# Kernel tuning notes

Hardware: AMD Instinct MI355X
Metric: run time of the kernel (lower is better)

The kernel has to match this reference:

```python
import jax, jax.numpy as jnp
import numpy as np

N = 16384   # nodes (atoms)
E = 262144  # edges (avg degree 16)
C = 64      # hidden channels per degree
H = 8       # attention heads
L = 4       # layers
R = 32      # radial MLP hidden
AED = 32    # atom embedding dim
TED = 32    # timestep embedding dim
NT = 1000   # num diffusion timesteps
NA = 16     # num atom types
DIN = AED + TED


def _sinusoidal(seq_len, dim):
    pos = np.arange(seq_len, dtype=np.float32)[:, None]
    dims = np.arange(dim, dtype=np.float32)[None, :]
    ang = pos / 10000.0 ** (2.0 * np.floor(dims / 2.0) / dim)
    emb = np.zeros((seq_len, dim), dtype=np.float32)
    emb[:, 0::2] = np.sin(ang[:, 0::2])
    emb[:, 1::2] = np.cos(ang[:, 1::2])
    return jnp.asarray(emb)


def setup_inputs() -> dict:
    key = jax.random.key(0)
    ks = jax.random.split(key, 20)
    def w(k, shape, fan_in):
        return jax.random.normal(k, shape, jnp.float32) / np.float32(np.sqrt(fan_in))
    return {
        'coordinates': jax.random.normal(ks[0], (N, 3), jnp.float32),
        'embed_table': w(ks[1], (NA, AED), 1.0),
        't_emb': _sinusoidal(NT, TED),
        'Win_s': w(ks[2], (DIN, C), DIN),
        'Win_v': w(ks[3], (1, C), 1.0),
        'Wq_s': w(ks[4], (L, C, C), C),
        'Wq_v': w(ks[5], (L, C, C), C),
        'Wk_s': w(ks[6], (L, C, C), C),
        'Wk_v': w(ks[7], (L, C, C), C),
        'R_W1': w(ks[8], (L, 1, R), 1.0),
        'R_b1': jnp.zeros((L, R), jnp.float32),
        'R_W2': w(ks[9], (L, R, H * 8), R),
        'R_b2': jnp.zeros((L, H * 8), jnp.float32),
        'Wo_s': w(ks[10], (L, C, C), C),
        'Wo_v': w(ks[11], (L, C, C), C),
        'Wout_v': w(ks[12], (C, 1), C),
        'atoms': jax.random.randint(ks[13], (N,), 0, NA),
        'src': jax.random.randint(ks[14], (E,), 0, N),
        'dst': jax.random.randint(ks[15], (E,), 0, N),
        't': 500,
    }


def _forward(coordinates, embed_table, t_emb, Win_s, Win_v, Wq_s, Wq_v, Wk_s, Wk_v,
             R_W1, R_b1, R_W2, R_b2, Wo_s, Wo_v, Wout_v, atoms, src, dst, t):
    n = coordinates.shape[0]
    Ch = C // H
    # center coordinates (as in wrapper)
    x = coordinates - coordinates.mean(axis=0, keepdims=True)
    # degree-0 input: atom embedding ++ timestep embedding
    s = jnp.concatenate([embed_table[atoms], jnp.broadcast_to(t_emb[t], (n, TED))], axis=-1)
    s = s @ Win_s                                        # [N, C] scalars
    # degree-1 input: coordinates (1 channel), lifted to C channels
    v = jnp.einsum('nkd,kc->ncd', x[:, None, :], Win_v)  # [N, C, 3] vectors
    # edge geometry (spherical-harmonic basis up to l=1: Y0=const, Y1 ~ rhat)
    rel = x[dst] - x[src]
    d = jnp.sqrt(jnp.sum(rel * rel, axis=-1) + 1e-12)    # [E]
    rhat = rel / d[:, None]                              # [E, 3]
    rh = rhat[:, None, None, :]                          # [E,1,1,3]
    for l in range(L):
        # radial network -> per-head CG-path weights (key/value x {0->0,1->0,1->1,0->1})
        rad = (jax.nn.relu(d[:, None] @ R_W1[l] + R_b1[l]) @ R_W2[l] + R_b2[l]).reshape(-1, H, 8)
        k_s = (s @ Wk_s[l])[src].reshape(-1, H, Ch)                          # [E,H,Ch]
        k_v = jnp.einsum('ecd,cf->efd', v[src], Wk_v[l]).reshape(-1, H, Ch, 3)
        vdotr = jnp.einsum('ehcd,ed->ehc', k_v, rhat)                        # 1x1 -> 0 path
        key_s = rad[..., 0:1] * k_s + rad[..., 1:2] * vdotr
        key_v = rad[..., 2:3, None] * k_v + rad[..., 3:4, None] * k_s[..., None] * rh
        val_s = rad[..., 4:5] * k_s + rad[..., 5:6] * vdotr
        val_v = rad[..., 6:7, None] * k_v + rad[..., 7:8, None] * k_s[..., None] * rh
        q_s = (s @ Wq_s[l]).reshape(n, H, Ch)[dst]
        q_v = jnp.einsum('ncd,cf->nfd', v, Wq_v[l]).reshape(n, H, Ch, 3)[dst]
        # invariant attention logits over incoming edges
        logit = ((q_s * key_s).sum(-1) + (q_v * key_v).sum((-1, -2))) / np.float32(np.sqrt(Ch))
        m = jax.lax.stop_gradient(jax.ops.segment_max(logit, dst, num_segments=n))
        a = jnp.exp(logit - m[dst])
        denom = jax.ops.segment_sum(a, dst, num_segments=n)
        alpha = a / (denom[dst] + 1e-9)                                      # [E,H]
        agg_s = jax.ops.segment_sum(alpha[..., None] * val_s, dst, num_segments=n).reshape(n, C)
        agg_v = jax.ops.segment_sum(alpha[..., None, None] * val_v, dst, num_segments=n).reshape(n, C, 3)
        # self-interaction + residual + equivariant nonlinearity
        s = jax.nn.silu(s + agg_s @ Wo_s[l])
        vr = v + jnp.einsum('ncd,cf->nfd', agg_v, Wo_v[l])
        v = vr * jax.nn.sigmoid(jnp.sum(vr * vr, axis=-1, keepdims=True))    # norm gate
    # fiber_out degree-1 with 1 channel -> updated coordinates
    return jnp.einsum('ncd,ck->nkd', v, Wout_v)[:, 0, :]                     # [N, 3]


def reference(coordinates, embed_table, t_emb, Win_s, Win_v, Wq_s, Wq_v, Wk_s, Wk_v,
              R_W1, R_b1, R_W2, R_b2, Wo_s, Wo_v, Wout_v, atoms, src, dst, t):
    return _forward(coordinates, embed_table, t_emb, Win_s, Win_v, Wq_s, Wq_v, Wk_s, Wk_v,
                    R_W1, R_b1, R_W2, R_b2, Wo_s, Wo_v, Wout_v, atoms, src, dst, t)
```

## Files before the change

kernel.cpp:

```cpp
#include <hip/hip_runtime.h>
#include <math.h>

#define NN 16384
#define NE 262144

constexpr size_t OFF_PART  = 0;
constexpr size_t OFF_MEAN  = 256;
constexpr size_t OFF_T     = 512;
constexpr size_t OFF_BIAS  = 1536;
constexpr size_t OFF_S     = 2048;
constexpr size_t OFF_V     = OFF_S     + (size_t)NN * 64;
constexpr size_t OFF_GEOM  = OFF_V     + (size_t)NN * 192;
constexpr size_t OFF_GEOMC = OFF_GEOM  + (size_t)NE * 4;
constexpr size_t OFF_QS    = OFF_GEOMC + (size_t)NE * 4;
constexpr size_t OFF_KS    = OFF_QS    + (size_t)NN * 64;
constexpr size_t OFF_QV    = OFF_KS    + (size_t)NN * 64;
constexpr size_t OFF_KV    = OFF_QV    + (size_t)NN * 192;
constexpr size_t OFF_RAD   = OFF_KV    + (size_t)NN * 192;
constexpr size_t OFF_INT   = OFF_RAD   + (size_t)NE * 64;
constexpr size_t I_ROWPTR  = OFF_INT;
constexpr size_t I_CURSOR  = OFF_INT + 16640;
constexpr size_t I_SRCC    = I_CURSOR + (size_t)NN;

static __device__ __forceinline__ double sigmoidd_(double x) {
  return 1.0 / (1.0 + exp(-x));
}

static __device__ __forceinline__ double fast_exp(double x) {
  x = fmax(x, -708.0);
  double y = x * 1.4426950408889634074;
  double k = rint(y);
  double r = fma(k, -6.93147180369123816490e-01, x);
  r = fma(k, -1.90821492927058770002e-10, r);
  double p = 2.755731922398589e-7;
  p = fma(p, r, 2.7557319223985893e-6);
  p = fma(p, r, 2.48015873015873016e-5);
  p = fma(p, r, 1.98412698412698413e-4);
  p = fma(p, r, 1.38888888888888889e-3);
  p = fma(p, r, 8.33333333333333333e-3);
  p = fma(p, r, 4.16666666666666667e-2);
  p = fma(p, r, 1.66666666666666667e-1);
  p = fma(p, r, 0.5);
  p = fma(p, r, 1.0);
  p = fma(p, r, 1.0);
  long long ki = (long long)k;
  double sc = __longlong_as_double((unsigned long long)(1023LL + ki) << 52);
  return p * sc;
}

__global__ void k_mean_partial(const float* __restrict__ coords, float* __restrict__ partials) {
  __shared__ double sm[3][256];
  int tid = threadIdx.x;
  int n = blockIdx.x * 256 + tid;
  sm[0][tid] = (double)coords[n * 3 + 0];
  sm[1][tid] = (double)coords[n * 3 + 1];
  sm[2][tid] = (double)coords[n * 3 + 2];
  __syncthreads();
  for (int off = 128; off > 0; off >>= 1) {
    if (tid < off) {
      sm[0][tid] += sm[0][tid + off];
      sm[1][tid] += sm[1][tid + off];
      sm[2][tid] += sm[2][tid + off];
    }
    __syncthreads();
  }
  if (tid == 0) {
    partials[blockIdx.x * 3 + 0] = (float)sm[0][0];
    partials[blockIdx.x * 3 + 1] = (float)sm[1][0];
    partials[blockIdx.x * 3 + 2] = (float)sm[2][0];
  }
}

__global__ void k_mean_final(const float* __restrict__ partials, float* __restrict__ mean) {
  int lane = threadIdx.x;
  double s0 = (double)partials[lane * 3 + 0];
  double s1 = (double)partials[lane * 3 + 1];
  double s2 = (double)partials[lane * 3 + 2];
  for (int off = 32; off > 0; off >>= 1) {
    s0 += __shfl_xor(s0, off);
    s1 += __shfl_xor(s1, off);
    s2 += __shfl_xor(s2, off);
  }
  if (lane == 0) {
    mean[0] = (float)(s0 * (1.0 / (double)NN));
    mean[1] = (float)(s1 * (1.0 / (double)NN));
    mean[2] = (float)(s2 * (1.0 / (double)NN));
  }
}

__global__ void k_prep_T(const float* __restrict__ embed, const float* __restrict__ t_emb,
                         const float* __restrict__ Win_s, const int* __restrict__ tptr,
                         float* __restrict__ T, float* __restrict__ bias) {
  int f = threadIdx.x;
  int tv = tptr[0];
  double b = 0.0;
  for (int k = 0; k < 32; ++k)
    b = fma((double)t_emb[tv * 32 + k], (double)Win_s[(32 + k) * 64 + f], b);
  bias[f] = (float)b;
  for (int a = 0; a < 16; ++a) {
    double acc = 0.0;
    for (int k = 0; k < 32; ++k)
      acc = fma((double)embed[a * 32 + k], (double)Win_s[k * 64 + f], acc);
    T[a * 64 + f] = (float)acc;
  }
}

__global__ void k_init_nodes(const float* __restrict__ coords, const float* __restrict__ mean,
                             const int* __restrict__ atoms, const float* __restrict__ T,
                             const float* __restrict__ bias, const float* __restrict__ Win_v,
                             float* __restrict__ S, float* __restrict__ V) {
  int id = blockIdx.x * 256 + threadIdx.x;
  int n = id >> 6, c = id & 63;
  double x0 = (double)coords[n * 3 + 0] - (double)mean[0];
  double x1 = (double)coords[n * 3 + 1] - (double)mean[1];
  double x2 = (double)coords[n * 3 + 2] - (double)mean[2];
  int a = atoms[n];
  S[n * 64 + c] = T[a * 64 + c] + bias[c];
  double w = (double)Win_v[c];
  V[(n * 64 + c) * 3 + 0] = (float)(x0 * w);
  V[(n * 64 + c) * 3 + 1] = (float)(x1 * w);
  V[(n * 64 + c) * 3 + 2] = (float)(x2 * w);
}

__global__ void k_edge_geom(const float* __restrict__ coords, const int* __restrict__ src,
                            const int* __restrict__ dst, float4* __restrict__ geom,
                            int* __restrict__ count) {
  int e = blockIdx.x * 256 + threadIdx.x;
  int se = src[e], de = dst[e];
  double rx = (double)coords[de * 3 + 0] - (double)coords[se * 3 + 0];
  double ry = (double)coords[de * 3 + 1] - (double)coords[se * 3 + 1];
  double rz = (double)coords[de * 3 + 2] - (double)coords[se * 3 + 2];
  double d2 = rx * rx + ry * ry + rz * rz + 1e-12;
  double dd = sqrt(d2);
  double inv = 1.0 / dd;
  geom[e] = make_float4((float)dd, (float)(rx * inv), (float)(ry * inv), (float)(rz * inv));
  atomicAdd(&count[de], 1);
}

__global__ void k_scan(int* count_cursor, int* rowptr) {
  __shared__ int buf[256];
  __shared__ int carry_s;
  int tid = threadIdx.x;
  if (tid == 0) carry_s = 0;
  __syncthreads();
  for (int base = 0; base < NN; base += 256) {
    int idx = base + tid;
    int val = count_cursor[idx];
    buf[tid] = val;
    __syncthreads();
    int incl = val;
    for (int off = 1; off < 256; off <<= 1) {
      int t = (tid >= off) ? buf[tid - off] : 0;
      __syncthreads();
      incl += t;
      buf[tid] = incl;
      __syncthreads();
    }
    int excl = carry_s + incl - val;
    rowptr[idx] = excl;
    count_cursor[idx] = excl;
    __syncthreads();
    if (tid == 255) carry_s += incl;
    __syncthreads();
  }
  if (tid == 0) rowptr[NN] = carry_s;
}

__global__ void k_scatter(const int* __restrict__ dst, const int* __restrict__ src,
                          const float4* __restrict__ geom, int* __restrict__ cursor,
                          int* __restrict__ srcc, float4* __restrict__ geomc) {
  int e = blockIdx.x * 256 + threadIdx.x;
  int de = dst[e];
  int pos = atomicAdd(&cursor[de], 1);
  srcc[pos] = src[e];
  geomc[pos] = geom[e];
}

__global__ void k_rad(const float4* __restrict__ geomc,
                      const float* __restrict__ R_W1, const float* __restrict__ R_b1,
                      const float* __restrict__ R_W2, const float* __restrict__ R_b2,
                      float* __restrict__ radc, int l) {
  __shared__ float2 w1b1[32];
  __shared__ float b2s[64];
  __shared__ float w2s[2048];
  for (int i = threadIdx.x; i < 2048; i += 256) w2s[i] = R_W2[l * 2048 + i];
  if (threadIdx.x < 64) b2s[threadIdx.x] = R_b2[l * 64 + threadIdx.x];
  if (threadIdx.x < 32)
    w1b1[threadIdx.x] = make_float2(R_W1[l * 32 + threadIdx.x], R_b1[l * 32 + threadIdx.x]);
  __syncthreads();
  int lane = threadIdx.x & 63;
  float w2col[32];
#pragma unroll
  for (int r = 0; r < 32; ++r) w2col[r] = w2s[r * 64 + lane];
  double b2v = (double)b2s[lane];
  float2 hwb = w1b1[lane & 31];
  for (int j = blockIdx.x * 4 + (threadIdx.x >> 6); j < NE; j += 4096) {
    float dd = geomc[j].x;
    double hd = fma((double)dd, (double)hwb.x, (double)hwb.y);
    float hidf = (float)fmax(hd, 0.0);
    double rad = b2v;
#pragma unroll
    for (int r = 0; r < 32; ++r)
      rad = fma((double)__shfl(hidf, r), (double)w2col[r], rad);
    radc[((size_t)j << 6) + lane] = (float)rad;
  }
}

__global__ void k_node_s(const float* __restrict__ S,
                         const float* __restrict__ Wq_s, const float* __restrict__ Wk_s,
                         float* __restrict__ QS, float* __restrict__ KS, int l) {
  __shared__ float wqs[4096], wks[4096];
  for (int i = threadIdx.x; i < 4096; i += 512) {
    wqs[i] = Wq_s[l * 4096 + i];
    wks[i] = Wk_s[l * 4096 + i];
  }
  __syncthreads();
  int lane = threadIdx.x & 63;
  for (int n = blockIdx.x * 8 + (threadIdx.x >> 6); n < NN; n += 8192) {
    float sv = S[n * 64 + lane];
    double aqs = 0.0, aks = 0.0;
#pragma unroll 8
    for (int c = 0; c < 64; ++c) {
      double sc = (double)__shfl(sv, c);
      aqs = fma(sc, (double)wqs[c * 64 + lane], aqs);
      aks = fma(sc, (double)wks[c * 64 + lane], aks);
    }
    QS[n * 64 + lane] = (float)aqs;
    KS[n * 64 + lane] = (float)aks;
  }
}

__global__ void k_node_v(const float* __restrict__ V,
                         const float* __restrict__ Wq_v, const float* __restrict__ Wk_v,
                         float* __restrict__ QV, float* __restrict__ KV, int l) {
  __shared__ float wqv[4096], wkv[4096];
  for (int i = threadIdx.x; i < 4096; i += 512) {
    wqv[i] = Wq_v[l * 4096 + i];
    wkv[i] = Wk_v[l * 4096 + i];
  }
  __syncthreads();
  int lane = threadIdx.x & 63;
  for (int n = blockIdx.x * 8 + (threadIdx.x >> 6); n < NN; n += 8192) {
    float v0 = V[(n * 64 + lane) * 3 + 0];
    float v1 = V[(n * 64 + lane) * 3 + 1];
    float v2 = V[(n * 64 + lane) * 3 + 2];
    double aqv0 = 0.0, aqv1 = 0.0, aqv2 = 0.0;
    double akv0 = 0.0, akv1 = 0.0, akv2 = 0.0;
#pragma unroll 8
    for (int c = 0; c < 64; ++c) {
      double u0 = (double)__shfl(v0, c);
      double u1 = (double)__shfl(v1, c);
      double u2 = (double)__shfl(v2, c);
      double wq = (double)wqv[c * 64 + lane];
      double wk = (double)wkv[c * 64 + lane];
      aqv0 = fma(u0, wq, aqv0); aqv1 = fma(u1, wq, aqv1); aqv2 = fma(u2, wq, aqv2);
      akv0 = fma(u0, wk, akv0); akv1 = fma(u1, wk, akv1); akv2 = fma(u2, wk, akv2);
    }
    QV[(n * 64 + lane) * 3 + 0] = (float)aqv0;
    QV[(n * 64 + lane) * 3 + 1] = (float)aqv1;
    QV[(n * 64 + lane) * 3 + 2] = (float)aqv2;
    KV[(n * 64 + lane) * 3 + 0] = (float)akv0;
    KV[(n * 64 + lane) * 3 + 1] = (float)akv1;
    KV[(n * 64 + lane) * 3 + 2] = (float)akv2;
  }
}

__global__ void k_aggregate(const float* __restrict__ QS, const float* __restrict__ KS,
                            const float* __restrict__ QV, const float* __restrict__ KV,
                            const float4* __restrict__ geomc, const float* __restrict__ radc,
                            const int* __restrict__ rowptr, const int* __restrict__ srcc,
                            const float* __restrict__ Wo_s, const float* __restrict__ Wo_v,
                            float* __restrict__ S, float* __restrict__ V, int l) {
  __shared__ float wos[4096];
  __shared__ float wov[4096];
  for (int i = threadIdx.x; i < 4096; i += 512) {
    wos[i] = Wo_s[l * 4096 + i];
    wov[i] = Wo_v[l * 4096 + i];
  }
  __syncthreads();
  int lane = threadIdx.x & 63;
  int gb = lane & 56;
  for (int n = blockIdx.x * 8 + (threadIdx.x >> 6); n < NN; n += 8192) {
    double qs = (double)QS[n * 64 + lane];
    double qv0 = (double)QV[(n * 64 + lane) * 3 + 0];
    double qv1 = (double)QV[(n * 64 + lane) * 3 + 1];
    double qv2 = (double)QV[(n * 64 + lane) * 3 + 2];
    int rb = rowptr[n], re = rowptr[n + 1];
    double m = -INFINITY, denom = 0.0;
    double as_ = 0.0, av0 = 0.0, av1 = 0.0, av2 = 0.0;
    for (int j = rb; j < re; ++j) {
      int se = srcc[j];
      float4 g = geomc[j];
      const float4* rp = (const float4*)(radc + ((size_t)j << 6) + gb);
      float4 rA = rp[0];
      float4 rB = rp[1];
      double rh0 = (double)g.y, rh1 = (double)g.z, rh2 = (double)g.w;
      double ksv = (double)KS[se * 64 + lane];
      double kv0 = (double)KV[(se * 64 + lane) * 3 + 0];
      double kv1 = (double)KV[(se * 64 + lane) * 3 + 1];
      double kv2 = (double)KV[(se * 64 + lane) * 3 + 2];
      double c0 = (double)rA.x, c1 = (double)rA.y, c2 = (double)rA.z, c3 = (double)rA.w;
      double c4 = (double)rB.x, c5 = (double)rB.y, c6 = (double)rB.z, c7 = (double)rB.w;
      double vdr = kv0 * rh0 + kv1 * rh1 + kv2 * rh2;
      double keys = c0 * ksv + c1 * vdr;
      double vals = c4 * ksv + c5 * vdr;
      double kx = c3 * ksv;
      double vx = c7 * ksv;
      double keyv0 = fma(c2, kv0, kx * rh0);
      double keyv1 = fma(c2, kv1, kx * rh1);
      double keyv2 = fma(c2, kv2, kx * rh2);
      double valv0 = fma(c6, kv0, vx * rh0);
      double valv1 = fma(c6, kv1, vx * rh1);
      double valv2 = fma(c6, kv2, vx * rh2);
      double lg = qs * keys + qv0 * keyv0 + qv1 * keyv1 + qv2 * keyv2;
      lg += __shfl_xor(lg, 1);
      lg += __shfl_xor(lg, 2);
      lg += __shfl_xor(lg, 4);
      lg *= 0.35355339059327376220;
      double nm = fmax(m, lg);
      double sc = fast_exp(m - nm);
      double a = fast_exp(lg - nm);
      m = nm;
      denom = fma(denom, sc, a);
      as_ = fma(as_, sc, a * vals);
      av0 = fma(av0, sc, a * valv0);
      av1 = fma(av1, sc, a * valv1);
      av2 = fma(av2, sc, a * valv2);
    }
    double inv = 1.0 / (denom + 1e-9);
    float aggs = (float)(as_ * inv);
    float agv0 = (float)(av0 * inv), agv1 = (float)(av1 * inv), agv2 = (float)(av2 * inv);
    double os = 0.0, ov0 = 0.0, ov1 = 0.0, ov2 = 0.0;
#pragma unroll 8
    for (int c = 0; c < 64; ++c) {
      double asc = (double)__shfl(aggs, c);
      double b0 = (double)__shfl(agv0, c);
      double b1 = (double)__shfl(agv1, c);
      double b2 = (double)__shfl(agv2, c);
      os = fma(asc, (double)wos[c * 64 + lane], os);
      double w = (double)wov[c * 64 + lane];
      ov0 = fma(b0, w, ov0); ov1 = fma(b1, w, ov1); ov2 = fma(b2, w, ov2);
    }
    double sn = (double)S[n * 64 + lane] + os;
    sn = sn * sigmoidd_(sn);
    S[n * 64 + lane] = (float)sn;
    double vr0 = (double)V[(n * 64 + lane) * 3 + 0] + ov0;
    double vr1 = (double)V[(n * 64 + lane) * 3 + 1] + ov1;
    double vr2 = (double)V[(n * 64 + lane) * 3 + 2] + ov2;
    double nrm = vr0 * vr0 + vr1 * vr1 + vr2 * vr2;
    double sg = sigmoidd_(nrm);
    V[(n * 64 + lane) * 3 + 0] = (float)(vr0 * sg);
    V[(n * 64 + lane) * 3 + 1] = (float)(vr1 * sg);
    V[(n * 64 + lane) * 3 + 2] = (float)(vr2 * sg);
  }
}

__global__ void k_output(const float* __restrict__ V, const float* __restrict__ Wout,
                         float* __restrict__ out) {
  int lane = threadIdx.x & 63;
  int n = blockIdx.x * 4 + (threadIdx.x >> 6);
  double w = (double)Wout[lane];
  double p0 = (double)V[(n * 64 + lane) * 3 + 0] * w;
  double p1 = (double)V[(n * 64 + lane) * 3 + 1] * w;
  double p2 = (double)V[(n * 64 + lane) * 3 + 2] * w;
  for (int off = 32; off > 0; off >>= 1) {
    p0 += __shfl_xor(p0, off);
    p1 += __shfl_xor(p1, off);
    p2 += __shfl_xor(p2, off);
  }
  if (lane == 0) {
    out[n * 3 + 0] = (float)p0;
    out[n * 3 + 1] = (float)p1;
    out[n * 3 + 2] = (float)p2;
  }
}

extern "C" void kernel_launch(void* const* d_in, const int* in_sizes, int n_in,
                              void* d_out, int out_size, void* d_ws, size_t ws_size,
                              hipStream_t stream) {
  (void)in_sizes; (void)n_in; (void)out_size; (void)ws_size;
  const float* coords = (const float*)d_in[0];
  const float* embed  = (const float*)d_in[1];
  const float* t_emb  = (const float*)d_in[2];
  const float* Win_s  = (const float*)d_in[3];
  const float* Win_v  = (const float*)d_in[4];
  const float* Wq_s   = (const float*)d_in[5];
  const float* Wq_v   = (const float*)d_in[6];
  const float* Wk_s   = (const float*)d_in[7];
  const float* Wk_v   = (const float*)d_in[8];
  const float* R_W1   = (const float*)d_in[9];
  const float* R_b1   = (const float*)d_in[10];
  const float* R_W2   = (const float*)d_in[11];
  const float* R_b2   = (const float*)d_in[12];
  const float* Wo_s   = (const float*)d_in[13];
  const float* Wo_v   = (const float*)d_in[14];
  const float* Wout_v = (const float*)d_in[15];
  const int* atoms = (const int*)d_in[16];
  const int* src   = (const int*)d_in[17];
  const int* dst   = (const int*)d_in[18];
  const int* tptr  = (const int*)d_in[19];

  float* ws    = (float*)d_ws;
  float* part  = ws + OFF_PART;
  float* mean  = ws + OFF_MEAN;
  float* Tp    = ws + OFF_T;
  float* bias  = ws + OFF_BIAS;
  float* Sp    = ws + OFF_S;
  float* Vp    = ws + OFF_V;
  float4* geom  = (float4*)(ws + OFF_GEOM);
  float4* geomc = (float4*)(ws + OFF_GEOMC);
  float* QSp   = ws + OFF_QS;
  float* KSp   = ws + OFF_KS;
  float* QVp   = ws + OFF_QV;
  float* KVp   = ws + OFF_KV;
  float* radc  = ws + OFF_RAD;
  int* rowptr = (int*)d_ws + I_ROWPTR;
  int* cursor = (int*)d_ws + I_CURSOR;
  int* srcc   = (int*)d_ws + I_SRCC;

  k_mean_partial<<<64, 256, 0, stream>>>(coords, part);
  k_mean_final<<<1, 64, 0, stream>>>(part, mean);
  k_prep_T<<<1, 64, 0, stream>>>(embed, t_emb, Win_s, tptr, Tp, bias);
  k_init_nodes<<<4096, 256, 0, stream>>>(coords, mean, atoms, Tp, bias, Win_v, Sp, Vp);

  hipMemsetAsync(cursor, 0, NN * sizeof(int), stream);
  k_edge_geom<<<NE / 256, 256, 0, stream>>>(coords, src, dst, geom, cursor);
  k_scan<<<1, 256, 0, stream>>>(cursor, rowptr);
  k_scatter<<<NE / 256, 256, 0, stream>>>(dst, src, geom, cursor, srcc, geomc);

  for (int l = 0; l < 4; ++l) {
    k_rad<<<1024, 256, 0, stream>>>(geomc, R_W1, R_b1, R_W2, R_b2, radc, l);
    k_node_s<<<1024, 512, 0, stream>>>(Sp, Wq_s, Wk_s, QSp, KSp, l);
    k_node_v<<<1024, 512, 0, stream>>>(Vp, Wq_v, Wk_v, QVp, KVp, l);
    k_aggregate<<<1024, 512, 0, stream>>>(QSp, KSp, QVp, KVp, geomc, radc, rowptr, srcc,
                                          Wo_s, Wo_v, Sp, Vp, l);
  }

  k_output<<<4096, 256, 0, stream>>>(Vp, Wout_v, (float*)d_out);
}
```

Before: 1.319 ms.

## Fuse per-layer prep kernels, parallelize CSR scan, interleave two nodes in aggregation

Merges the radial MLP and the scalar and vector Q/K projection kernels into one launch, splitting blocks by role, which cuts launches and lets the three workloads overlap. Replaces the single-block serial scan with a three-stage multi-block scan. The aggregation kernel now processes two nodes per wave with interleaved edge loops to expose more memory-level parallelism, at the cost of higher register pressure and imbalance when the two degrees differ. The radial weights are pre-converted to double in registers.

```diff
diff --git a/kernel.cpp b/kernel.cpp
--- a/kernel.cpp
+++ b/kernel.cpp
@@ -137,33 +137,43 @@
   atomicAdd(&count[de], 1);
 }
 
-__global__ void k_scan(int* count_cursor, int* rowptr) {
+__global__ void k_scan1(const int* __restrict__ count, int* __restrict__ rowptr,
+                        int* __restrict__ bsum) {
   __shared__ int buf[256];
-  __shared__ int carry_s;
-  int tid = threadIdx.x;
-  if (tid == 0) carry_s = 0;
+  int tid = threadIdx.x, idx = blockIdx.x * 256 + tid;
+  int val = count[idx];
+  buf[tid] = val;
   __syncthreads();
-  for (int base = 0; base < NN; base += 256) {
-    int idx = base + tid;
-    int val = count_cursor[idx];
-    buf[tid] = val;
+  int incl = val;
+  for (int off = 1; off < 256; off <<= 1) {
+    int t = (tid >= off) ? buf[tid - off] : 0;
     __syncthreads();
-    int incl = val;
-    for (int off = 1; off < 256; off <<= 1) {
-      int t = (tid >= off) ? buf[tid - off] : 0;
-      __syncthreads();
-      incl += t;
-      buf[tid] = incl;
-      __syncthreads();
-    }
-    int excl = carry_s + incl - val;
-    rowptr[idx] = excl;
-    count_cursor[idx] = excl;
+    incl += t;
+    buf[tid] = incl;
     __syncthreads();
-    if (tid == 255) carry_s += incl;
-    __syncthreads();
-  }
-  if (tid == 0) rowptr[NN] = carry_s;
+  }
+  rowptr[idx] = incl - val;
+  if (tid == 255) bsum[blockIdx.x] = incl;
+}
+
+__global__ void k_scan2(int* __restrict__ bsum, int* __restrict__ rowptr) {
+  int lane = threadIdx.x;
+  int v = bsum[lane];
+  int incl = v;
+  for (int off = 1; off < 64; off <<= 1) {
+    int t = __shfl_up(incl, off);
+    if (lane >= off) incl += t;
+  }
+  bsum[lane] = incl - v;
+  if (lane == 63) rowptr[NN] = incl;
+}
+
+__global__ void k_scan3(int* __restrict__ rowptr, int* __restrict__ cursor,
+                        const int* __restrict__ bsum) {
+  int idx = blockIdx.x * 256 + threadIdx.x;
+  int v = rowptr[idx] + bsum[blockIdx.x];
+  rowptr[idx] = v;
+  cursor[idx] = v;
 }
 
 __global__ void k_scatter(const int* __restrict__ dst, const int* __restrict__ src,
@@ -176,101 +186,158 @@
   geomc[pos] = geom[e];
 }
 
-__global__ void k_rad(const float4* __restrict__ geomc,
-                      const float* __restrict__ R_W1, const float* __restrict__ R_b1,
-                      const float* __restrict__ R_W2, const float* __restrict__ R_b2,
-                      float* __restrict__ radc, int l) {
-  __shared__ float2 w1b1[32];
-  __shared__ float b2s[64];
-  __shared__ float w2s[2048];
-  for (int i = threadIdx.x; i < 2048; i += 256) w2s[i] = R_W2[l * 2048 + i];
-  if (threadIdx.x < 64) b2s[threadIdx.x] = R_b2[l * 64 + threadIdx.x];
-  if (threadIdx.x < 32)
-    w1b1[threadIdx.x] = make_float2(R_W1[l * 32 + threadIdx.x], R_b1[l * 32 + threadIdx.x]);
-  __syncthreads();
+#define RAD_B 512
+#define NV_B  384
+__global__ __launch_bounds__(512) void k_layer_pre(
+    const float4* __restrict__ geomc,
+    const float* __restrict__ R_W1, const float* __restrict__ R_b1,
+    const float* __restrict__ R_W2, const float* __restrict__ R_b2,
+    float* __restrict__ radc,
+    const float* __restrict__ S,
+    const float* __restrict__ Wq_s, const float* __restrict__ Wk_s,
+    float* __restrict__ QS, float* __restrict__ KS,
+    const float* __restrict__ V,
+    const float* __restrict__ Wq_v, const float* __restrict__ Wk_v,
+    float* __restrict__ QV, float* __restrict__ KV, int l) {
+  __shared__ float smem[8192];
   int lane = threadIdx.x & 63;
-  float w2col[32];
+  int wv = threadIdx.x >> 6;
+  if (blockIdx.x < RAD_B) {
+    float* w2s = smem;
+    float* b2s = smem + 2048;
+    float2* w1b1 = (float2*)(smem + 2112);
+    for (int i = threadIdx.x; i < 2048; i += 512) w2s[i] = R_W2[l * 2048 + i];
+    if (threadIdx.x < 64) b2s[threadIdx.x] = R_b2[l * 64 + threadIdx.x];
+    if (threadIdx.x < 32)
+      w1b1[threadIdx.x] = make_float2(R_W1[l * 32 + threadIdx.x], R_b1[l * 32 + threadIdx.x]);
+    __syncthreads();
+    double w2d[32];
 #pragma unroll
-  for (int r = 0; r < 32; ++r) w2col[r] = w2s[r * 64 + lane];
-  double b2v = (double)b2s[lane];
-  float2 hwb = w1b1[lane & 31];
-  for (int j = blockIdx.x * 4 + (threadIdx.x >> 6); j < NE; j += 4096) {
-    float dd = geomc[j].x;
-    double hd = fma((double)dd, (double)hwb.x, (double)hwb.y);
-    float hidf = (float)fmax(hd, 0.0);
-    double rad = b2v;
+    for (int r = 0; r < 32; ++r) w2d[r] = (double)w2s[r * 64 + lane];
+    double b2v = (double)b2s[lane];
+    float2 hwb = w1b1[lane & 31];
+    int j0 = blockIdx.x * 8 + wv;
+    for (int j = j0; j < NE; j += 4096) {
+      float dd = geomc[j].x;
+      double hd = fma((double)dd, (double)hwb.x, (double)hwb.y);
+      float hidf = (float)fmax(hd, 0.0);
+      double rad = b2v;
 #pragma unroll
-    for (int r = 0; r < 32; ++r)
-      rad = fma((double)__shfl(hidf, r), (double)w2col[r], rad);
-    radc[((size_t)j << 6) + lane] = (float)rad;
-  }
-}
-
-__global__ void k_node_s(const float* __restrict__ S,
-                         const float* __restrict__ Wq_s, const float* __restrict__ Wk_s,
-                         float* __restrict__ QS, float* __restrict__ KS, int l) {
-  __shared__ float wqs[4096], wks[4096];
-  for (int i = threadIdx.x; i < 4096; i += 512) {
-    wqs[i] = Wq_s[l * 4096 + i];
-    wks[i] = Wk_s[l * 4096 + i];
-  }
-  __syncthreads();
-  int lane = threadIdx.x & 63;
-  for (int n = blockIdx.x * 8 + (threadIdx.x >> 6); n < NN; n += 8192) {
-    float sv = S[n * 64 + lane];
-    double aqs = 0.0, aks = 0.0;
+      for (int r = 0; r < 32; ++r)
+        rad = fma((double)__shfl(hidf, r), w2d[r], rad);
+      radc[((size_t)j << 6) + lane] = (float)rad;
+    }
+  } else if (blockIdx.x < RAD_B + NV_B) {
+    float* wqv = smem;
+    float* wkv = smem + 4096;
+    for (int i = threadIdx.x; i < 4096; i += 512) {
+      wqv[i] = Wq_v[l * 4096 + i];
+      wkv[i] = Wk_v[l * 4096 + i];
+    }
+    __syncthreads();
+    int slot = (blockIdx.x - RAD_B) * 8 + wv;
+    for (int n = slot; n < NN; n += 3072) {
+      float v0 = V[(n * 64 + lane) * 3 + 0];
+      float v1 = V[(n * 64 + lane) * 3 + 1];
+      float v2 = V[(n * 64 + lane) * 3 + 2];
+      double aqv0 = 0.0, aqv1 = 0.0, aqv2 = 0.0;
+      double akv0 = 0.0, akv1 = 0.0, akv2 = 0.0;
 #pragma unroll 8
-    for (int c = 0; c < 64; ++c) {
-      double sc = (double)__shfl(sv, c);
-      aqs = fma(sc, (double)wqs[c * 64 + lane], aqs);
-      aks = fma(sc, (double)wks[c * 64 + lane], aks);
+      for (int c = 0; c < 64; ++c) {
+        double u0 = (double)__shfl(v0, c);
+        double u1 = (double)__shfl(v1, c);
+        double u2 = (double)__shfl(v2, c);
+        double wq = (double)wqv[c * 64 + lane];
+        double wk = (double)wkv[c * 64 + lane];
+        aqv0 = fma(u0, wq, aqv0); aqv1 = fma(u1, wq, aqv1); aqv2 = fma(u2, wq, aqv2);
+        akv0 = fma(u0, wk, akv0); akv1 = fma(u1, wk, akv1); akv2 = fma(u2, wk, akv2);
+      }
+      QV[(n * 64 + lane) * 3 + 0] = (float)aqv0;
+      QV[(n * 64 + lane) * 3 + 1] = (float)aqv1;
+      QV[(n * 64 + lane) * 3 + 2] = (float)aqv2;
+      KV[(n * 64 + lane) * 3 + 0] = (float)akv0;
+      KV[(n * 64 + lane) * 3 + 1] = (float)akv1;
+      KV[(n * 64 + lane) * 3 + 2] = (float)akv2;
     }
-    QS[n * 64 + lane] = (float)aqs;
-    KS[n * 64 + lane] = (float)aks;
-  }
-}
-
-__global__ void k_node_v(const float* __restrict__ V,
-                         const float* __restrict__ Wq_v, const float* __restrict__ Wk_v,
-                         float* __restrict__ QV, float* __restrict__ KV, int l) {
-  __shared__ float wqv[4096], wkv[4096];
-  for (int i = threadIdx.x; i < 4096; i += 512) {
-    wqv[i] = Wq_v[l * 4096 + i];
-    wkv[i] = Wk_v[l * 4096 + i];
-  }
-  __syncthreads();
-  int lane = threadIdx.x & 63;
-  for (int n = blockIdx.x * 8 + (threadIdx.x >> 6); n < NN; n += 8192) {
-    float v0 = V[(n * 64 + lane) * 3 + 0];
-    float v1 = V[(n * 64 + lane) * 3 + 1];
-    float v2 = V[(n * 64 + lane) * 3 + 2];
-    double aqv0 = 0.0, aqv1 = 0.0, aqv2 = 0.0;
-    double akv0 = 0.0, akv1 = 0.0, akv2 = 0.0;
+  } else {
+    float* wqs = smem;
+    float* wks = smem + 4096;
+    for (int i = threadIdx.x; i < 4096; i += 512) {
+      wqs[i] = Wq_s[l * 4096 + i];
+      wks[i] = Wk_s[l * 4096 + i];
+    }
+    __syncthreads();
+    int slot = (blockIdx.x - RAD_B - NV_B) * 8 + wv;
+    for (int n = slot; n < NN; n += 1024) {
+      float sv = S[n * 64 + lane];
+      double aqs = 0.0, aks = 0.0;
 #pragma unroll 8
-    for (int c = 0; c < 64; ++c) {
-      double u0 = (double)__shfl(v0, c);
-      double u1 = (double)__shfl(v1, c);
-      double u2 = (double)__shfl(v2, c);
-      double wq = (double)wqv[c * 64 + lane];
-      double wk = (double)wkv[c * 64 + lane];
-      aqv0 = fma(u0, wq, aqv0); aqv1 = fma(u1, wq, aqv1); aqv2 = fma(u2, wq, aqv2);
-      akv0 = fma(u0, wk, akv0); akv1 = fma(u1, wk, akv1); akv2 = fma(u2, wk, akv2);
+      for (int c = 0; c < 64; ++c) {
+        double sc = (double)__shfl(sv, c);
+        aqs = fma(sc, (double)wqs[c * 64 + lane], aqs);
+        aks = fma(sc, (double)wks[c * 64 + lane], aks);
+      }
+      QS[n * 64 + lane] = (float)aqs;
+      KS[n * 64 + lane] = (float)aks;
     }
-    QV[(n * 64 + lane) * 3 + 0] = (float)aqv0;
-    QV[(n * 64 + lane) * 3 + 1] = (float)aqv1;
-    QV[(n * 64 + lane) * 3 + 2] = (float)aqv2;
-    KV[(n * 64 + lane) * 3 + 0] = (float)akv0;
-    KV[(n * 64 + lane) * 3 + 1] = (float)akv1;
-    KV[(n * 64 + lane) * 3 + 2] = (float)akv2;
-  }
-}
-
-__global__ void k_aggregate(const float* __restrict__ QS, const float* __restrict__ KS,
-                            const float* __restrict__ QV, const float* __restrict__ KV,
-                            const float4* __restrict__ geomc, const float* __restrict__ radc,
-                            const int* __restrict__ rowptr, const int* __restrict__ srcc,
-                            const float* __restrict__ Wo_s, const float* __restrict__ Wo_v,
-                            float* __restrict__ S, float* __restrict__ V, int l) {
+  }
+}
+
+struct Acc {
+  double m, den, as, av0, av1, av2;
+  double qs, qv0, qv1, qv2;
+};
+
+static __device__ __forceinline__ void edge_step(
+    int j, int lane, int gb,
+    const float* __restrict__ KS, const float* __restrict__ KV,
+    const float4* __restrict__ geomc, const float* __restrict__ radc,
+    const int* __restrict__ srcc, Acc& A) {
+  int se = srcc[j];
+  float4 g = geomc[j];
+  const float4* rp = (const float4*)(radc + ((size_t)j << 6) + gb);
+  float4 rA = rp[0], rB = rp[1];
+  double rh0 = (double)g.y, rh1 = (double)g.z, rh2 = (double)g.w;
+  double ksv = (double)KS[se * 64 + lane];
+  double kv0 = (double)KV[(se * 64 + lane) * 3 + 0];
+  double kv1 = (double)KV[(se * 64 + lane) * 3 + 1];
+  double kv2 = (double)KV[(se * 64 + lane) * 3 + 2];
+  double c0 = (double)rA.x, c1 = (double)rA.y, c2 = (double)rA.z, c3 = (double)rA.w;
+  double c4 = (double)rB.x, c5 = (double)rB.y, c6 = (double)rB.z, c7 = (double)rB.w;
+  double vdr = kv0 * rh0 + kv1 * rh1 + kv2 * rh2;
+  double keys = c0 * ksv + c1 * vdr;
+  double vals = c4 * ksv + c5 * vdr;
+  double kx = c3 * ksv;
+  double vx = c7 * ksv;
+  double keyv0 = fma(c2, kv0, kx * rh0);
+  double keyv1 = fma(c2, kv1, kx * rh1);
+  double keyv2 = fma(c2, kv2, kx * rh2);
+  double valv0 = fma(c6, kv0, vx * rh0);
+  double valv1 = fma(c6, kv1, vx * rh1);
+  double valv2 = fma(c6, kv2, vx * rh2);
+  double lg = A.qs * keys + A.qv0 * keyv0 + A.qv1 * keyv1 + A.qv2 * keyv2;
+  lg += __shfl_xor(lg, 1);
+  lg += __shfl_xor(lg, 2);
+  lg += __shfl_xor(lg, 4);
+  lg *= 0.35355339059327376220;
+  double nm = fmax(A.m, lg);
+  double sc = fast_exp(A.m - nm);
+  double a = fast_exp(lg - nm);
+  A.m = nm;
+  A.den = fma(A.den, sc, a);
+  A.as  = fma(A.as,  sc, a * vals);
+  A.av0 = fma(A.av0, sc, a * valv0);
+  A.av1 = fma(A.av1, sc, a * valv1);
+  A.av2 = fma(A.av2, sc, a * valv2);
+}
+
+__global__ __launch_bounds__(512) void k_aggregate(
+    const float* __restrict__ QS, const float* __restrict__ KS,
+    const float* __restrict__ QV, const float* __restrict__ KV,
+    const float4* __restrict__ geomc, const float* __restrict__ radc,
+    const int* __restrict__ rowptr, const int* __restrict__ srcc,
+    const float* __restrict__ Wo_s, const float* __restrict__ Wo_v,
+    float* __restrict__ S, float* __restrict__ V, int l) {
   __shared__ float wos[4096];
   __shared__ float wov[4096];
   for (int i = threadIdx.x; i < 4096; i += 512) {
@@ -280,78 +347,78 @@
   __syncthreads();
   int lane = threadIdx.x & 63;
   int gb = lane & 56;
-  for (int n = blockIdx.x * 8 + (threadIdx.x >> 6); n < NN; n += 8192) {
-    double qs = (double)QS[n * 64 + lane];
-    double qv0 = (double)QV[(n * 64 + lane) * 3 + 0];
-    double qv1 = (double)QV[(n * 64 + lane) * 3 + 1];
-    double qv2 = (double)QV[(n * 64 + lane) * 3 + 2];
-    int rb = rowptr[n], re = rowptr[n + 1];
-    double m = -INFINITY, denom = 0.0;
-    double as_ = 0.0, av0 = 0.0, av1 = 0.0, av2 = 0.0;
-    for (int j = rb; j < re; ++j) {
-      int se = srcc[j];
-      float4 g = geomc[j];
-      const float4* rp = (const float4*)(radc + ((size_t)j << 6) + gb);
-      float4 rA = rp[0];
-      float4 rB = rp[1];
-      double rh0 = (double)g.y, rh1 = (double)g.z, rh2 = (double)g.w;
-      double ksv = (double)KS[se * 64 + lane];
-      double kv0 = (double)KV[(se * 64 + lane) * 3 + 0];
-      double kv1 = (double)KV[(se * 64 + lane) * 3 + 1];
-      double kv2 = (double)KV[(se * 64 + lane) * 3 + 2];
-      double c0 = (double)rA.x, c1 = (double)rA.y, c2 = (double)rA.z, c3 = (double)rA.w;
-      double c4 = (double)rB.x, c5 = (double)rB.y, c6 = (double)rB.z, c7 = (double)rB.w;
-      double vdr = kv0 * rh0 + kv1 * rh1 + kv2 * rh2;
-      double keys = c0 * ksv + c1 * vdr;
-      double vals = c4 * ksv + c5 * vdr;
-      double kx = c3 * ksv;
-      double vx = c7 * ksv;
-      double keyv0 = fma(c2, kv0, kx * rh0);
-      double keyv1 = fma(c2, kv1, kx * rh1);
-      double keyv2 = fma(c2, kv2, kx * rh2);
-      double valv0 = fma(c6, kv0, vx * rh0);
-      double valv1 = fma(c6, kv1, vx * rh1);
-      double valv2 = fma(c6, kv2, vx * rh2);
-      double lg = qs * keys + qv0 * keyv0 + qv1 * keyv1 + qv2 * keyv2;
-      lg += __shfl_xor(lg, 1);
-      lg += __shfl_xor(lg, 2);
-      lg += __shfl_xor(lg, 4);
-      lg *= 0.35355339059327376220;
-      double nm = fmax(m, lg);
-      double sc = fast_exp(m - nm);
-      double a = fast_exp(lg - nm);
-      m = nm;
-      denom = fma(denom, sc, a);
-      as_ = fma(as_, sc, a * vals);
-      av0 = fma(av0, sc, a * valv0);
-      av1 = fma(av1, sc, a * valv1);
-      av2 = fma(av2, sc, a * valv2);
-    }
-    double inv = 1.0 / (denom + 1e-9);
-    float aggs = (float)(as_ * inv);
-    float agv0 = (float)(av0 * inv), agv1 = (float)(av1 * inv), agv2 = (float)(av2 * inv);
-    double os = 0.0, ov0 = 0.0, ov1 = 0.0, ov2 = 0.0;
+  int n0 = blockIdx.x * 8 + (threadIdx.x >> 6);
+  int n1 = n0 + 8192;
+  Acc A0, A1;
+  A0.qs = (double)QS[n0 * 64 + lane];
+  A0.qv0 = (double)QV[(n0 * 64 + lane) * 3 + 0];
+  A0.qv1 = (double)QV[(n0 * 64 + lane) * 3 + 1];
+  A0.qv2 = (double)QV[(n0 * 64 + lane) * 3 + 2];
+  A1.qs = (double)QS[n1 * 64 + lane];
+  A1.qv0 = (double)QV[(n1 * 64 + lane) * 3 + 0];
+  A1.qv1 = (double)QV[(n1 * 64 + lane) * 3 + 1];
+  A1.qv2 = (double)QV[(n1 * 64 + lane) * 3 + 2];
+  A0.m = -INFINITY; A0.den = 0.0; A0.as = 0.0; A0.av0 = 0.0; A0.av1 = 0.0; A0.av2 = 0.0;
+  A1.m = -INFINITY; A1.den = 0.0; A1.as = 0.0; A1.av0 = 0.0; A1.av1 = 0.0; A1.av2 = 0.0;
+  int j0 = rowptr[n0], e0 = rowptr[n0 + 1];
+  int j1 = rowptr[n1], e1 = rowptr[n1 + 1];
+  while (j0 < e0 && j1 < e1) {
+    edge_step(j0, lane, gb, KS, KV, geomc, radc, srcc, A0);
+    edge_step(j1, lane, gb, KS, KV, geomc, radc, srcc, A1);
+    ++j0; ++j1;
+  }
+  while (j0 < e0) { edge_step(j0, lane, gb, KS, KV, geomc, radc, srcc, A0); ++j0; }
+  while (j1 < e1) { edge_step(j1, lane, gb, KS, KV, geomc, radc, srcc, A1); ++j1; }
+  double inv0 = 1.0 / (A0.den + 1e-9);
+  double inv1 = 1.0 / (A1.den + 1e-9);
+  float aggs0 = (float)(A0.as * inv0);
+  float agv00 = (float)(A0.av0 * inv0), agv01 = (float)(A0.av1 * inv0), agv02 = (float)(A0.av2 * inv0);
+  float aggs1 = (float)(A1.as * inv1);
+  float agv10 = (float)(A1.av0 * inv1), agv11 = (float)(A1.av1 * inv1), agv12 = (float)(A1.av2 * inv1);
+  double os0 = 0.0, ov00 = 0.0, ov01 = 0.0, ov02 = 0.0;
+  double os1 = 0.0, ov10 = 0.0, ov11 = 0.0, ov12 = 0.0;
 #pragma unroll 8
-    for (int c = 0; c < 64; ++c) {
-      double asc = (double)__shfl(aggs, c);
-      double b0 = (double)__shfl(agv0, c);
-      double b1 = (double)__shfl(agv1, c);
-      double b2 = (double)__shfl(agv2, c);
-      os = fma(asc, (double)wos[c * 64 + lane], os);
-      double w = (double)wov[c * 64 + lane];
-      ov0 = fma(b0, w, ov0); ov1 = fma(b1, w, ov1); ov2 = fma(b2, w, ov2);
-    }
-    double sn = (double)S[n * 64 + lane] + os;
+  for (int c = 0; c < 64; ++c) {
+    double wsv = (double)wos[c * 64 + lane];
+    double wvv = (double)wov[c * 64 + lane];
+    double a0 = (double)__shfl(aggs0, c);
+    double b00 = (double)__shfl(agv00, c);
+    double b01 = (double)__shfl(agv01, c);
+    double b02 = (double)__shfl(agv02, c);
+    os0 = fma(a0, wsv, os0);
+    ov00 = fma(b00, wvv, ov00); ov01 = fma(b01, wvv, ov01); ov02 = fma(b02, wvv, ov02);
+    double a1 = (double)__shfl(aggs1, c);
+    double b10 = (double)__shfl(agv10, c);
+    double b11 = (double)__shfl(agv11, c);
+    double b12 = (double)__shfl(agv12, c);
+    os1 = fma(a1, wsv, os1);
+    ov10 = fma(b10, wvv, ov10); ov11 = fma(b11, wvv, ov11); ov12 = fma(b12, wvv, ov12);
+  }
+  {
+    double sn = (double)S[n0 * 64 + lane] + os0;
     sn = sn * sigmoidd_(sn);
-    S[n * 64 + lane] = (float)sn;
-    double vr0 = (double)V[(n * 64 + lane) * 3 + 0] + ov0;
-    double vr1 = (double)V[(n * 64 + lane) * 3 + 1] + ov1;
-    double vr2 = (double)V[(n * 64 + lane) * 3 + 2] + ov2;
+    S[n0 * 64 + lane] = (float)sn;
+    double vr0 = (double)V[(n0 * 64 + lane) * 3 + 0] + ov00;
+    double vr1 = (double)V[(n0 * 64 + lane) * 3 + 1] + ov01;
+    double vr2 = (double)V[(n0 * 64 + lane) * 3 + 2] + ov02;
     double nrm = vr0 * vr0 + vr1 * vr1 + vr2 * vr2;
     double sg = sigmoidd_(nrm);
-    V[(n * 64 + lane) * 3 + 0] = (float)(vr0 * sg);
-    V[(n * 64 + lane) * 3 + 1] = (float)(vr1 * sg);
-    V[(n * 64 + lane) * 3 + 2] = (float)(vr2 * sg);
+    V[(n0 * 64 + lane) * 3 + 0] = (float)(vr0 * sg);
+    V[(n0 * 64 + lane) * 3 + 1] = (float)(vr1 * sg);
+    V[(n0 * 64 + lane) * 3 + 2] = (float)(vr2 * sg);
+  }
+  {
+    double sn = (double)S[n1 * 64 + lane] + os1;
+    sn = sn * sigmoidd_(sn);
+    S[n1 * 64 + lane] = (float)sn;
+    double vr0 = (double)V[(n1 * 64 + lane) * 3 + 0] + ov10;
+    double vr1 = (double)V[(n1 * 64 + lane) * 3 + 1] + ov11;
+    double vr2 = (double)V[(n1 * 64 + lane) * 3 + 2] + ov12;
+    double nrm = vr0 * vr0 + vr1 * vr1 + vr2 * vr2;
+    double sg = sigmoidd_(nrm);
+    V[(n1 * 64 + lane) * 3 + 0] = (float)(vr0 * sg);
+    V[(n1 * 64 + lane) * 3 + 1] = (float)(vr1 * sg);
+    V[(n1 * 64 + lane) * 3 + 2] = (float)(vr2 * sg);
   }
 }
 
@@ -414,6 +481,7 @@
   float* QVp   = ws + OFF_QV;
   float* KVp   = ws + OFF_KV;
   float* radc  = ws + OFF_RAD;
+  int* bsum   = (int*)d_ws + OFF_PART;
   int* rowptr = (int*)d_ws + I_ROWPTR;
   int* cursor = (int*)d_ws + I_CURSOR;
   int* srcc   = (int*)d_ws + I_SRCC;
@@ -425,13 +493,15 @@
 
   hipMemsetAsync(cursor, 0, NN * sizeof(int), stream);
   k_edge_geom<<<NE / 256, 256, 0, stream>>>(coords, src, dst, geom, cursor);
-  k_scan<<<1, 256, 0, stream>>>(cursor, rowptr);
+  k_scan1<<<64, 256, 0, stream>>>(cursor, rowptr, bsum);
+  k_scan2<<<1, 64, 0, stream>>>(bsum, rowptr);
+  k_scan3<<<64, 256, 0, stream>>>(rowptr, cursor, bsum);
   k_scatter<<<NE / 256, 256, 0, stream>>>(dst, src, geom, cursor, srcc, geomc);
 
   for (int l = 0; l < 4; ++l) {
-    k_rad<<<1024, 256, 0, stream>>>(geomc, R_W1, R_b1, R_W2, R_b2, radc, l);
-    k_node_s<<<1024, 512, 0, stream>>>(Sp, Wq_s, Wk_s, QSp, KSp, l);
-    k_node_v<<<1024, 512, 0, stream>>>(Vp, Wq_v, Wk_v, QVp, KVp, l);
+    k_layer_pre<<<1024, 512, 0, stream>>>(geomc, R_W1, R_b1, R_W2, R_b2, radc,
+                                          Sp, Wq_s, Wk_s, QSp, KSp,
+                                          Vp, Wq_v, Wk_v, QVp, KVp, l);
     k_aggregate<<<1024, 512, 0, stream>>>(QSp, KSp, QVp, KVp, geomc, radc, rowptr, srcc,
                                           Wo_s, Wo_v, Sp, Vp, l);
   }
```

Result: slower. 1.828 ms (+38.6%).
